# Kernel optimization log

Measured on AMD Instinct MI355X. Metric: run time of the kernel, lower is better.

Reference implementation:

```python
import jax, jax.numpy as jnp
import numpy as np

ALPHA = 0.8
WIN = 11
SIGMA = 1.5
DATA_RANGE = 1.0
K1, K2 = 0.01, 0.03


def _gaussian_kernel(size, sigma):
    coords = jnp.arange(size, dtype=jnp.float32) - size // 2
    g = jnp.exp(-coords ** 2 / (2.0 * sigma ** 2))
    k = jnp.outer(g, g)
    return k / jnp.sum(k)


def _depthwise_conv(x, kernel):
    # x: (B, C, H, W); kernel: (C, 1, K, K); groups=C, SAME padding (pad=K//2)
    C = x.shape[1]
    pad = kernel.shape[-1] // 2
    return jax.lax.conv_general_dilated(
        x, kernel,
        window_strides=(1, 1),
        padding=[(pad, pad), (pad, pad)],
        dimension_numbers=('NCHW', 'OIHW', 'NCHW'),
        feature_group_count=C,
    )


def _ssim(pred, target):
    C1 = (K1 * DATA_RANGE) ** 2
    C2 = (K2 * DATA_RANGE) ** 2
    channels = pred.shape[1]
    k2d = _gaussian_kernel(WIN, SIGMA)
    kernel = jnp.broadcast_to(k2d[None, None], (channels, 1, WIN, WIN))

    conv = lambda t: _depthwise_conv(t, kernel)
    mu_x = conv(pred)
    mu_y = conv(target)
    mu_x2, mu_y2, mu_xy = mu_x ** 2, mu_y ** 2, mu_x * mu_y
    sigma_x2 = conv(pred * pred) - mu_x2
    sigma_y2 = conv(target * target) - mu_y2
    sigma_xy = conv(pred * target) - mu_xy
    numerator = (2.0 * mu_xy + C1) * (2.0 * sigma_xy + C2)
    denominator = (mu_x2 + mu_y2 + C1) * (sigma_x2 + sigma_y2 + C2)
    return jnp.mean(numerator / denominator)


def setup_inputs() -> dict:
    key = jax.random.key(0)
    k1, k2 = jax.random.split(key)
    shape = (32, 3, 512, 512)
    pred = jax.random.uniform(k1, shape, dtype=jnp.float32)
    target = jax.random.uniform(k2, shape, dtype=jnp.float32)
    return {"pred": pred, "target": target}


def reference(pred, target):
    mse_loss = jnp.mean((pred - target) ** 2)
    ssim_loss = 1.0 - _ssim(jnp.clip(pred, 0.0, 1.0), target)
    return ALPHA * mse_loss + (1.0 - ALPHA) * ssim_loss
```

## Files before the change

### kernel.cpp

```cpp
#include <hip/hip_runtime.h>
#include <hip/hip_fp16.h>


#define W 512
#define H 512
#define NIMG 96
#define TX 64
#define CHUNK 16
#define STRIP 128
#define NITER 8
#define BUF 26
#define PADH 66
#define NSLOT 128
#define RAWB 10240

typedef __fp16 h2 __attribute__((ext_vector_type(2)));

#define GW(k)  gwu[(k) < 6 ? (k) : 10 - (k)]
#define GWH(k) gwh[(k) < 6 ? (k) : 10 - (k)]

#define GLL(sp, dp) __builtin_amdgcn_global_load_lds(                         \
    (const __attribute__((address_space(1))) void*)(sp),                      \
    (__attribute__((address_space(3))) void*)(dp), 16, 0, 0)

__global__ void hybrid_init(double* __restrict__ ws) {
    int t = threadIdx.x;
    if (t < 2 * NSLOT) ws[t] = 0.0;
}

__global__ __launch_bounds__(256, 4) void hybrid_main(
    const float* __restrict__ pred, const float* __restrict__ targ,
    double* __restrict__ ws)
{
    __shared__ uint2 s_q[BUF][PADH];
    __shared__ __align__(16) char s_raw[RAWB];

    const int tid = threadIdx.x;
    const float* __restrict__ pp = pred + (size_t)blockIdx.z * (H * W);
    const float* __restrict__ tp = targ + (size_t)blockIdx.z * (H * W);
    const int xbase = blockIdx.x * TX;
    const int Y0 = blockIdx.y * STRIP;
    const int xb8 = xbase - 8;

    float gwu[6];
    __fp16 gwh[6];
    {
        float s = 0.f;
#pragma unroll
        for (int k = 0; k < 6; ++k) {
            float d = (float)(k - 5);
            gwu[k] = expf(-d * d / 4.5f);
            s += (k < 5) ? 2.f * gwu[k] : gwu[k];
        }
        float inv = 1.f / s;
#pragma unroll
        for (int k = 0; k < 6; ++k) { gwu[k] *= inv; gwh[k] = (__fp16)gwu[k]; }
    }

    const int hrow_i = (tid >> 4) & 15;
    const int g      = tid & 15;
    const int c0     = g * 4;
    const int A0     = xbase + c0 - 8;
    const bool inX   = (A0 >= 0) && (A0 + 20 <= W);

    const int wv     = (tid >> 6) & 3;
    const int cc     = tid & 63;
    const int lane16 = (tid & 63) * 16;

    const bool tb = ((int)blockIdx.z == NIMG - 1) && ((int)blockIdx.y == (H / STRIP) - 1);

    float mse_local = 0.f, ssim_local = 0.f;

    auto mkaddr = [&](int m, const float*& sp, const char*& dp) {
        const int t  = (m >= 5);
        const int mm = m - 5 * t;
        const int oo = mm * 1024 + lane16;
        const int r  = oo / 320;
        const int cb = oo - r * 320;
        int col = xb8 + (cb >> 2);
        col = col < 0 ? 0 : (col > W - 4 ? W - 4 : col);
        sp = (t ? tp : pp) + (size_t)(Y0 + 5 + r) * W + col;
        dp = s_raw + m * 1024;
    };
    const float *sA, *sB, *sC = nullptr;
    const char  *dA, *dB, *dC = nullptr;
    mkaddr(wv, sA, dA);
    mkaddr(wv + 4, sB, dB);
    const bool hasC = (wv + 8) < 10;
    if (hasC) mkaddr(wv + 8, sC, dC);

    auto issue_fast = [&]() {
        GLL(sA, dA); sA += CHUNK * W;
        GLL(sB, dB); sB += CHUNK * W;
        if (hasC) { GLL(sC, dC); sC += CHUNK * W; }
    };

    auto issue_slow = [&](int kc) {
        const int gybase = Y0 + 5 + CHUNK * kc;
#pragma unroll
        for (int m0 = 0; m0 < 12; m0 += 4) {
            const int m = wv + m0;
            if (m < 10) {
                const int t  = (m >= 5);
                const int oo = (m - 5 * t) * 1024 + lane16;
                const int r  = oo / 320;
                const int cb = oo - r * 320;
                int gy = gybase + r; if (gy > H - 1) gy = H - 1;
                int col = xb8 + (cb >> 2);
                col = col < 0 ? 0 : (col > W - 4 ? W - 4 : col);
                const float* src = (t ? tp : pp) + gy * W + col;
                GLL(src, s_raw + m * 1024);
            }
        }
    };

    auto read_staged = [&](float* xa, float* ya) {
#pragma unroll
        for (int v = 0; v < 5; ++v) {
            const int off = hrow_i * 320 + (g + v) * 16;
            float4 a = *(const float4*)&s_raw[off];
            float4 b = *(const float4*)&s_raw[RAWB / 2 + off];
            xa[4*v+0]=a.x; xa[4*v+1]=a.y; xa[4*v+2]=a.z; xa[4*v+3]=a.w;
            ya[4*v+0]=b.x; ya[4*v+1]=b.y; ya[4*v+2]=b.z; ya[4*v+3]=b.w;
        }
        if (!inX) {
#pragma unroll
            for (int j = 0; j < 20; ++j) {
                if ((unsigned)(A0 + j) >= (unsigned)W) { xa[j] = 0.f; ya[j] = 0.f; }
            }
        }
    };

    auto hconv_store = [&](const float* xa, const float* ya, int slot, bool own) {
        if (own) {
#pragma unroll
            for (int c = 0; c < 4; ++c) {
                float d = xa[8 + c] - ya[8 + c];
                mse_local = fmaf(d, d, mse_local);
            }
        }
        h2 a01[4], a2x[4];
#pragma unroll
        for (int i = 0; i < 4; ++i) {
            a01[i] = (h2)(__fp16)0.f;
            a2x[i] = (h2)(__fp16)0.f;
        }
#pragma unroll
        for (int j = 0; j < 14; ++j) {
            float cx = __builtin_amdgcn_fmed3f(xa[3 + j], 0.f, 1.f);
            float yv = ya[3 + j];
            float s2 = fmaf(yv, yv, cx * cx);
            float xy = cx * yv;
            h2 p0 = __builtin_amdgcn_cvt_pkrtz(cx, yv);
            h2 p1 = __builtin_amdgcn_cvt_pkrtz(s2, xy);
#pragma unroll
            for (int i = 0; i < 4; ++i) {
                int k = j - i;
                if (k >= 0 && k < 11) {
                    __fp16 w = GWH(k);
                    h2 w2; w2.x = w; w2.y = w;
                    a01[i] = w2 * p0 + a01[i];
                    a2x[i] = w2 * p1 + a2x[i];
                }
            }
        }
#pragma unroll
        for (int i = 0; i < 4; ++i) {
            uint2 u;
            u.x = __builtin_bit_cast(unsigned int, a01[i]);
            u.y = __builtin_bit_cast(unsigned int, a2x[i]);
            s_q[slot][c0 + i] = u;
        }
    };

    if (tb) issue_slow(0); else issue_fast();
    if (hrow_i < 10) {
        float xa[20], ya[20];
        const int gy = Y0 - 5 + hrow_i;
        if (gy >= 0 && gy < H) {
            const float* __restrict__ px = pp + (size_t)gy * W;
            const float* __restrict__ py = tp + (size_t)gy * W;
            if (inX) {
                const float4* qx = (const float4*)(px + A0);
                const float4* qy = (const float4*)(py + A0);
#pragma unroll
                for (int v = 0; v < 5; ++v) {
                    float4 a = qx[v], b = qy[v];
                    xa[4*v+0]=a.x; xa[4*v+1]=a.y; xa[4*v+2]=a.z; xa[4*v+3]=a.w;
                    ya[4*v+0]=b.x; ya[4*v+1]=b.y; ya[4*v+2]=b.z; ya[4*v+3]=b.w;
                }
            } else {
#pragma unroll
                for (int j = 0; j < 20; ++j) {
                    int col = A0 + j;
                    bool ok = (col >= 0) && (col < W);
                    xa[j] = ok ? px[col] : 0.f;
                    ya[j] = ok ? py[col] : 0.f;
                }
            }
        } else {
#pragma unroll
            for (int j = 0; j < 20; ++j) { xa[j] = 0.f; ya[j] = 0.f; }
        }
        hconv_store(xa, ya, hrow_i, hrow_i >= 5);
    }
    __syncthreads();

    const float C1 = 1e-4f, C2 = 9e-4f;

#pragma unroll
    for (int k = 0; k < NITER; ++k) {
        {
            const int ext = CHUNK * k + 10 + hrow_i;
            const int gy  = Y0 - 5 + ext;
            const int hb  = (10 + CHUNK * k) % BUF;
            int slot;
            if (hb + 15 >= BUF) {
                slot = hb + hrow_i; if (slot >= BUF) slot -= BUF;
            } else {
                slot = hb + hrow_i;
            }
            if (gy < H) {
                float xa[20], ya[20];
                read_staged(xa, ya);
                hconv_store(xa, ya, slot, ext <= STRIP + 4);
            } else {
                uint2 z; z.x = 0u; z.y = 0u;
#pragma unroll
                for (int i = 0; i < 4; ++i) s_q[slot][c0 + i] = z;
            }
        }
        __syncthreads();

        if (k + 1 < NITER) { if (tb) issue_slow(k + 1); else issue_fast(); }

        {
            const int vb = (CHUNK * k) % BUF;
            const int r4 = 4 * wv;
            h2 a01[4], a2x[4];
#pragma unroll
            for (int i = 0; i < 4; ++i) {
                a01[i] = (h2)(__fp16)0.f;
                a2x[i] = (h2)(__fp16)0.f;
            }
#pragma unroll
            for (int j = 0; j < 14; ++j) {
                const int sj = vb + j;
                int s;
                if (sj + 12 >= BUF) {
                    s = sj + r4; if (s >= BUF) s -= BUF;
                } else {
                    s = sj + r4;
                }
                uint2 u = s_q[s][cc];
                h2 lo = __builtin_bit_cast(h2, u.x);
                h2 hi = __builtin_bit_cast(h2, u.y);
#pragma unroll
                for (int i = 0; i < 4; ++i) {
                    int kk = j - i;
                    if (kk >= 0 && kk < 11) {
                        __fp16 w = GWH(kk);
                        h2 w2; w2.x = w; w2.y = w;
                        a01[i] = w2 * lo + a01[i];
                        a2x[i] = w2 * hi + a2x[i];
                    }
                }
            }
#pragma unroll
            for (int i = 0; i < 4; ++i) {
                float mux = (float)a01[i].x, muy = (float)a01[i].y;
                float es  = (float)a2x[i].x, exy = (float)a2x[i].y;
                float mu_x2 = mux * mux, mu_y2 = muy * muy, mu_xy = mux * muy;
                float ssum = es - mu_x2 - mu_y2;
                float sxy  = exy - mu_xy;
                float num = (2.f*mu_xy + C1) * (2.f*sxy + C2);
                float den = (mu_x2 + mu_y2 + C1) * (ssum + C2);
                ssim_local = fmaf(num, __builtin_amdgcn_rcpf(den), ssim_local);
            }
        }
        __syncthreads();
    }

    float m = mse_local, s2 = ssim_local;
#pragma unroll
    for (int off = 32; off; off >>= 1) {
        m  += __shfl_down(m, off);
        s2 += __shfl_down(s2, off);
    }
    if ((tid & 63) == 0) {
        int flat = blockIdx.x + 8 * (blockIdx.y + 4 * blockIdx.z);
        int slot = (flat * 4 + wv) & (NSLOT - 1);
        atomicAdd(&ws[slot], (double)m);
        atomicAdd(&ws[NSLOT + slot], (double)s2);
    }
}

__global__ void hybrid_fin(const double* __restrict__ ws, float* __restrict__ out) {
    int t = threadIdx.x;
    double m = ws[t] + ws[t + 64];
    double s = ws[NSLOT + t] + ws[NSLOT + t + 64];
#pragma unroll
    for (int off = 32; off; off >>= 1) {
        m += __shfl_down(m, off);
        s += __shfl_down(s, off);
    }
    if (t == 0) {
        const double N = (double)NIMG * H * W;
        double mse  = m / N;
        double ssim = s / N;
        out[0] = (float)(0.8 * mse + 0.2 * (1.0 - ssim));
    }
}

extern "C" void kernel_launch(void* const* d_in, const int* in_sizes, int n_in,
                              void* d_out, int out_size, void* d_ws, size_t ws_size,
                              hipStream_t stream) {
    const float* pred = (const float*)d_in[0];
    const float* targ = (const float*)d_in[1];
    double* ws = (double*)d_ws;
    float* out = (float*)d_out;

    hybrid_init<<<1, 256, 0, stream>>>(ws);
    dim3 grid(W / TX, H / STRIP, NIMG);
    hybrid_main<<<grid, dim3(256), 0, stream>>>(pred, targ, ws);
    hybrid_fin<<<1, 64, 0, stream>>>(ws, out);
}
```

Baseline: 90.34 us.

## Double-buffer the raw LDS staging and prefetch the next chunk earlier

Splits the raw staging LDS buffer into two halves. The next chunk's global_load_lds prefetch is now issued at the top of each iteration, before the current chunk is read and horizontally convolved. The mid-iteration __syncthreads is replaced by an LDS-only waitcnt plus s_barrier, so in-flight global loads are not drained there. This is meant to hide global-load latency behind the hconv and vconv work, at the cost of 10KB more LDS per block and reliance on correct vmcnt waits elsewhere.

New measurement: 95.38 us. 5.6% more time.

```diff
diff --git a/kernel.cpp b/kernel.cpp
--- a/kernel.cpp
+++ b/kernel.cpp
@@ -33,7 +33,7 @@
     double* __restrict__ ws)
 {
     __shared__ uint2 s_q[BUF][PADH];
-    __shared__ __align__(16) char s_raw[RAWB];
+    __shared__ __align__(16) char s_raw[2][RAWB];
 
     const int tid = threadIdx.x;
     const float* __restrict__ pp = pred + (size_t)blockIdx.z * (H * W);
@@ -71,7 +71,7 @@
 
     float mse_local = 0.f, ssim_local = 0.f;
 
-    auto mkaddr = [&](int m, const float*& sp, const char*& dp) {
+    auto mksrc = [&](int m, const float*& sp) {
         const int t  = (m >= 5);
         const int mm = m - 5 * t;
         const int oo = mm * 1024 + lane16;
@@ -80,22 +80,21 @@
         int col = xb8 + (cb >> 2);
         col = col < 0 ? 0 : (col > W - 4 ? W - 4 : col);
         sp = (t ? tp : pp) + (size_t)(Y0 + 5 + r) * W + col;
-        dp = s_raw + m * 1024;
     };
     const float *sA, *sB, *sC = nullptr;
-    const char  *dA, *dB, *dC = nullptr;
-    mkaddr(wv, sA, dA);
-    mkaddr(wv + 4, sB, dB);
+    mksrc(wv, sA);
+    mksrc(wv + 4, sB);
     const bool hasC = (wv + 8) < 10;
-    if (hasC) mkaddr(wv + 8, sC, dC);
-
-    auto issue_fast = [&]() {
-        GLL(sA, dA); sA += CHUNK * W;
-        GLL(sB, dB); sB += CHUNK * W;
-        if (hasC) { GLL(sC, dC); sC += CHUNK * W; }
-    };
-
-    auto issue_slow = [&](int kc) {
+    if (hasC) mksrc(wv + 8, sC);
+    const int oA = wv * 1024, oB = (wv + 4) * 1024, oC = (wv + 8) * 1024;
+
+    auto issue_fast = [&](int par) {
+        GLL(sA, &s_raw[par][oA]); sA += CHUNK * W;
+        GLL(sB, &s_raw[par][oB]); sB += CHUNK * W;
+        if (hasC) { GLL(sC, &s_raw[par][oC]); sC += CHUNK * W; }
+    };
+
+    auto issue_slow = [&](int kc, int par) {
         const int gybase = Y0 + 5 + CHUNK * kc;
 #pragma unroll
         for (int m0 = 0; m0 < 12; m0 += 4) {
@@ -109,17 +108,17 @@
                 int col = xb8 + (cb >> 2);
                 col = col < 0 ? 0 : (col > W - 4 ? W - 4 : col);
                 const float* src = (t ? tp : pp) + gy * W + col;
-                GLL(src, s_raw + m * 1024);
-            }
-        }
-    };
-
-    auto read_staged = [&](float* xa, float* ya) {
+                GLL(src, &s_raw[par][m * 1024]);
+            }
+        }
+    };
+
+    auto read_staged = [&](const char* base, float* xa, float* ya) {
 #pragma unroll
         for (int v = 0; v < 5; ++v) {
             const int off = hrow_i * 320 + (g + v) * 16;
-            float4 a = *(const float4*)&s_raw[off];
-            float4 b = *(const float4*)&s_raw[RAWB / 2 + off];
+            float4 a = *(const float4*)&base[off];
+            float4 b = *(const float4*)&base[RAWB / 2 + off];
             xa[4*v+0]=a.x; xa[4*v+1]=a.y; xa[4*v+2]=a.z; xa[4*v+3]=a.w;
             ya[4*v+0]=b.x; ya[4*v+1]=b.y; ya[4*v+2]=b.z; ya[4*v+3]=b.w;
         }
@@ -173,7 +172,7 @@
         }
     };
 
-    if (tb) issue_slow(0); else issue_fast();
+    if (tb) issue_slow(0, 0); else issue_fast(0);
     if (hrow_i < 10) {
         float xa[20], ya[20];
         const int gy = Y0 - 5 + hrow_i;
@@ -210,6 +209,9 @@
 
 #pragma unroll
     for (int k = 0; k < NITER; ++k) {
+        if (k + 1 < NITER) {
+            if (tb) issue_slow(k + 1, (k + 1) & 1); else issue_fast((k + 1) & 1);
+        }
         {
             const int ext = CHUNK * k + 10 + hrow_i;
             const int gy  = Y0 - 5 + ext;
@@ -222,7 +224,7 @@
             }
             if (gy < H) {
                 float xa[20], ya[20];
-                read_staged(xa, ya);
+                read_staged(s_raw[k & 1], xa, ya);
                 hconv_store(xa, ya, slot, ext <= STRIP + 4);
             } else {
                 uint2 z; z.x = 0u; z.y = 0u;
@@ -230,9 +232,9 @@
                 for (int i = 0; i < 4; ++i) s_q[slot][c0 + i] = z;
             }
         }
-        __syncthreads();
-
-        if (k + 1 < NITER) { if (tb) issue_slow(k + 1); else issue_fast(); }
+        asm volatile("s_waitcnt lgkmcnt(0)" ::: "memory");
+        __builtin_amdgcn_s_barrier();
+        __builtin_amdgcn_sched_barrier(0);
 
         {
             const int vb = (CHUNK * k) % BUF;
```
